# Kernel tuning notes

Measured on AMD Instinct MI355X. Metric: run time of the kernel, lower is better.

Reference implementation:

```python
import jax, jax.numpy as jnp
import numpy as np

MODEL_DIM = 1024
BATCH, SEQ = 4, 2048


def setup_inputs() -> dict:
    key = jax.random.key(0)
    kx, kq, kk, kv = jax.random.split(key, 4)
    s = 1.0 / np.sqrt(MODEL_DIM)
    return {
        "x": jax.random.normal(kx, (BATCH, SEQ, MODEL_DIM), dtype=jnp.float32),
        "Wq": jax.random.normal(kq, (MODEL_DIM, MODEL_DIM), dtype=jnp.float32) * s,
        "Wk": jax.random.normal(kk, (MODEL_DIM, MODEL_DIM), dtype=jnp.float32) * s,
        "Wv": jax.random.normal(kv, (MODEL_DIM, MODEL_DIM), dtype=jnp.float32) * s,
    }


def reference(x, Wq, Wk, Wv):
    # nn.Linear(d, d, bias=False): y = x @ W.T ; W stored [out, in]
    q = jnp.einsum("bsd,ed->bse", x, Wq)
    k = jnp.einsum("bsd,ed->bse", x, Wk)
    v = jnp.einsum("bsd,ed->bse", x, Wv)
    scores = jnp.einsum("bqd,bkd->bqk", q, k) / jnp.sqrt(jnp.float32(MODEL_DIM))
    attn = jax.nn.softmax(scores, axis=-1)
    return jnp.einsum("bqk,bkd->bqd", attn, v)
```

## Files before the change

kernel.cpp:

```cpp
#include <hip/hip_runtime.h>
#include <hip/hip_bf16.h>


typedef short bf16x8_t __attribute__((ext_vector_type(8)));
typedef float f32x4_t __attribute__((ext_vector_type(4)));
typedef unsigned short u16x8_t __attribute__((ext_vector_type(8)));

static __device__ __forceinline__ unsigned short f2bf(float f) {
  __hip_bfloat16 h = __float2bfloat16(f);
  return *reinterpret_cast<unsigned short*>(&h);
}
static __device__ __forceinline__ float bf2f(unsigned short u) {
  return __uint_as_float(((unsigned int)u) << 16);
}

#define GLOAD_LDS16(gp, lp)                                            \
  __builtin_amdgcn_global_load_lds(                                    \
      (const __attribute__((address_space(1))) void*)(gp),             \
      (__attribute__((address_space(3))) void*)(lp), 16, 0, 0)

__global__ __launch_bounds__(256) void cast_f32_bf16(
    const float* __restrict__ in, unsigned short* __restrict__ out, int n8) {
  int i = blockIdx.x * 256 + threadIdx.x;
  if (i >= n8) return;
  float4 a = ((const float4*)in)[i * 2];
  float4 b = ((const float4*)in)[i * 2 + 1];
  u16x8_t o;
  o[0] = f2bf(a.x);
  o[1] = f2bf(a.y);
  o[2] = f2bf(a.z);
  o[3] = f2bf(a.w);
  o[4] = f2bf(b.x);
  o[5] = f2bf(b.y);
  o[6] = f2bf(b.z);
  o[7] = f2bf(b.w);
  ((u16x8_t*)out)[i] = o;
}

template <bool OUT_BF16, int BN>
__global__ __launch_bounds__(256) void gemm_nt(
    const unsigned short* __restrict__ A, const unsigned short* __restrict__ B,
    void* __restrict__ Cv, int M, int N, int K, int lda, int ldb, int ldc,
    long long sA, long long sB, long long sC, float alpha) {
  constexpr int NB = BN / 32;
  __shared__ unsigned short As[128 * 64];
  __shared__ unsigned short Bs[BN * 64];

  const int gx = gridDim.x, gy = gridDim.y;
  const int nwg = gx * gy * gridDim.z;
  const int orig = (blockIdx.z * gy + blockIdx.y) * gx + blockIdx.x;
  const int swz = (orig & 7) * (nwg >> 3) + (orig >> 3);
  const int bx = swz % gx;
  const int tmp = swz / gx;
  const int by = tmp % gy;
  const int z = tmp / gy;

  const int tid = threadIdx.x;
  const int lane = tid & 63;
  const int w = tid >> 6;
  const int wm = w >> 1, wn = w & 1;
  const int m0 = by * 128;
  const int n0 = bx * BN;

  A += (long long)z * sA;
  B += (long long)z * sB;

  int sarow[4], sacol[4];
#pragma unroll
  for (int i = 0; i < 4; ++i) {
    int p = w * 256 + i * 64 + lane;
    int r = p >> 3;
    int c8 = (p & 7) ^ (r & 7);
    sarow[i] = r;
    sacol[i] = c8 * 8;
  }
  int sbrow[NB], sbcol[NB];
#pragma unroll
  for (int i = 0; i < NB; ++i) {
    int p = w * (BN * 2) + i * 64 + lane;
    int r = p >> 3;
    int c8 = (p & 7) ^ (r & 7);
    sbrow[i] = r;
    sbcol[i] = c8 * 8;
  }

  const int q = lane >> 4, rl = lane & 15;
  int aoff[4][2], boff[NB][2];
#pragma unroll
  for (int t = 0; t < 4; ++t) {
#pragma unroll
    for (int ks = 0; ks < 2; ++ks) {
      int ra = wm * 64 + t * 16 + rl;
      int ca = ks * 4 + q;
      aoff[t][ks] = ra * 64 + ((ca ^ (ra & 7)) * 8);
    }
  }
#pragma unroll
  for (int u = 0; u < NB; ++u) {
#pragma unroll
    for (int ks = 0; ks < 2; ++ks) {
      int rb = wn * (BN / 2) + u * 16 + rl;
      int ca = ks * 4 + q;
      boff[u][ks] = rb * 64 + ((ca ^ (rb & 7)) * 8);
    }
  }

  f32x4_t acc[4][NB];
#pragma unroll
  for (int i = 0; i < 4; ++i)
#pragma unroll
    for (int j = 0; j < NB; ++j) acc[i][j] = (f32x4_t){0.f, 0.f, 0.f, 0.f};

  for (int k0 = 0; k0 < K; k0 += 64) {
    __syncthreads();
#pragma unroll
    for (int i = 0; i < 4; ++i) {
      GLOAD_LDS16(&A[(long long)(m0 + sarow[i]) * lda + k0 + sacol[i]],
                  &As[(w * 4 + i) * 512]);
    }
#pragma unroll
    for (int i = 0; i < NB; ++i) {
      GLOAD_LDS16(&B[(long long)(n0 + sbrow[i]) * ldb + k0 + sbcol[i]],
                  &Bs[(w * NB + i) * 512]);
    }
    __syncthreads();

#pragma unroll
    for (int ks = 0; ks < 2; ++ks) {
      bf16x8_t af[4], bg[NB];
#pragma unroll
      for (int t = 0; t < 4; ++t) af[t] = *(const bf16x8_t*)&As[aoff[t][ks]];
#pragma unroll
      for (int u = 0; u < NB; ++u) bg[u] = *(const bf16x8_t*)&Bs[boff[u][ks]];
#pragma unroll
      for (int i = 0; i < 4; ++i)
#pragma unroll
        for (int j = 0; j < NB; ++j)
          acc[i][j] = __builtin_amdgcn_mfma_f32_16x16x32_bf16(af[i], bg[j],
                                                              acc[i][j], 0, 0, 0);
    }
  }

  if (OUT_BF16) {
    unsigned short* C = (unsigned short*)Cv + (long long)z * sC;
#pragma unroll
    for (int t = 0; t < 4; ++t)
#pragma unroll
      for (int u = 0; u < NB; ++u)
#pragma unroll
        for (int j = 0; j < 4; ++j) {
          int row = m0 + wm * 64 + t * 16 + q * 4 + j;
          int col = n0 + wn * (BN / 2) + u * 16 + rl;
          C[(long long)row * ldc + col] = f2bf(acc[t][u][j] * alpha);
        }
  } else {
    float* C = (float*)Cv + (long long)z * sC;
#pragma unroll
    for (int t = 0; t < 4; ++t)
#pragma unroll
      for (int u = 0; u < NB; ++u)
#pragma unroll
        for (int j = 0; j < 4; ++j) {
          int row = m0 + wm * 64 + t * 16 + q * 4 + j;
          int col = n0 + wn * (BN / 2) + u * 16 + rl;
          C[(long long)row * ldc + col] = acc[t][u][j] * alpha;
        }
  }
}

__global__ __launch_bounds__(256) void softmax_bf16(
    unsigned short* __restrict__ S) {
  unsigned short* p = S + (long long)blockIdx.x * 2048;
  const int tid = threadIdx.x;

  u16x8_t v = ((u16x8_t*)p)[tid];
  float f[8];
#pragma unroll
  for (int j = 0; j < 8; ++j) f[j] = bf2f(v[j]);

  float m = f[0];
#pragma unroll
  for (int j = 1; j < 8; ++j) m = fmaxf(m, f[j]);
#pragma unroll
  for (int off = 32; off > 0; off >>= 1) m = fmaxf(m, __shfl_xor(m, off));

  __shared__ float redm[4];
  __shared__ float reds[4];
  if ((tid & 63) == 0) redm[tid >> 6] = m;
  __syncthreads();
  m = fmaxf(fmaxf(redm[0], redm[1]), fmaxf(redm[2], redm[3]));

  float s = 0.f;
#pragma unroll
  for (int j = 0; j < 8; ++j) {
    f[j] = __expf(f[j] - m);
    s += f[j];
  }
#pragma unroll
  for (int off = 32; off > 0; off >>= 1) s += __shfl_xor(s, off);
  if ((tid & 63) == 0) reds[tid >> 6] = s;
  __syncthreads();
  s = (reds[0] + reds[1]) + (reds[2] + reds[3]);

  const float inv = 1.0f / s;
#pragma unroll
  for (int j = 0; j < 8; ++j) v[j] = f2bf(f[j] * inv);
  ((u16x8_t*)p)[tid] = v;
}

extern "C" void kernel_launch(void* const* d_in, const int* in_sizes, int n_in,
                              void* d_out, int out_size, void* d_ws,
                              size_t ws_size, hipStream_t stream) {
  const float* x = (const float*)d_in[0];
  const float* Wq = (const float*)d_in[1];
  const float* Wk = (const float*)d_in[2];
  const float* Wv = (const float*)d_in[3];
  float* out = (float*)d_out;

  unsigned short* xb = (unsigned short*)d_ws;
  unsigned short* Wqb = xb + 8388608;
  unsigned short* Wkb = Wqb + 1048576;
  unsigned short* Wvb = Wkb + 1048576;
  unsigned short* Qb = Wvb + 1048576;
  unsigned short* Kb = Qb + 8388608;
  unsigned short* VTb = Kb + 8388608;
  unsigned short* Scb = VTb + 8388608;

  const dim3 blk(256);

  cast_f32_bf16<<<4096, blk, 0, stream>>>(x, xb, 1048576);
  cast_f32_bf16<<<512, blk, 0, stream>>>(Wq, Wqb, 131072);
  cast_f32_bf16<<<512, blk, 0, stream>>>(Wk, Wkb, 131072);
  cast_f32_bf16<<<512, blk, 0, stream>>>(Wv, Wvb, 131072);

  gemm_nt<true, 128><<<dim3(8, 64, 2), blk, 0, stream>>>(
      xb, Wqb, Qb, 8192, 1024, 1024, 1024, 1024, 1024, 0, 1048576,
      8388608, 1.0f);
  gemm_nt<true, 128><<<dim3(64, 8, 1), blk, 0, stream>>>(
      Wvb, xb, VTb, 1024, 8192, 1024, 1024, 1024, 8192, 0, 0, 0, 1.0f);

  gemm_nt<true, 128><<<dim3(16, 16, 4), blk, 0, stream>>>(
      Qb, Kb, Scb, 2048, 2048, 1024, 1024, 1024, 2048, (long long)2048 * 1024,
      (long long)2048 * 1024, (long long)2048 * 2048, 0.03125f);

  softmax_bf16<<<8192, blk, 0, stream>>>(Scb);

  gemm_nt<false, 64><<<dim3(16, 16, 4), blk, 0, stream>>>(
      Scb, VTb, out, 2048, 1024, 2048, 2048, 8192, 1024,
      (long long)2048 * 2048, 2048, (long long)2048 * 1024, 1.0f);
}
```

Measured before the change: 194.6 us.

## Fuse softmax into QK^T epilogue, batch Q/K projection, add 256-tile double-buffered GEMM

Drops the separate softmax kernel. The QK^T GEMM epilogue now writes exp(scores) as bf16 and atomically adds row sums, and the PV GEMM divides by those sums. Q and K projections are merged into one 256x256-tile GEMM with a concatenated weight matrix, and the three weight casts are merged into one launch. The new GEMM uses 512 threads with a two-stage global-to-LDS pipeline and MFMA priority hints. The risk is that softmax no longer subtracts the row max, so exp can overflow for inputs with large scores. It also adds float atomics on the row sums.

```diff
diff --git a/kernel.cpp b/kernel.cpp
--- a/kernel.cpp
+++ b/kernel.cpp
@@ -9,9 +9,6 @@
 static __device__ __forceinline__ unsigned short f2bf(float f) {
   __hip_bfloat16 h = __float2bfloat16(f);
   return *reinterpret_cast<unsigned short*>(&h);
-}
-static __device__ __forceinline__ float bf2f(unsigned short u) {
-  return __uint_as_float(((unsigned int)u) << 16);
 }
 
 #define GLOAD_LDS16(gp, lp)                                            \
@@ -26,25 +23,41 @@
   float4 a = ((const float4*)in)[i * 2];
   float4 b = ((const float4*)in)[i * 2 + 1];
   u16x8_t o;
-  o[0] = f2bf(a.x);
-  o[1] = f2bf(a.y);
-  o[2] = f2bf(a.z);
-  o[3] = f2bf(a.w);
-  o[4] = f2bf(b.x);
-  o[5] = f2bf(b.y);
-  o[6] = f2bf(b.z);
-  o[7] = f2bf(b.w);
+  o[0] = f2bf(a.x); o[1] = f2bf(a.y); o[2] = f2bf(a.z); o[3] = f2bf(a.w);
+  o[4] = f2bf(b.x); o[5] = f2bf(b.y); o[6] = f2bf(b.z); o[7] = f2bf(b.w);
   ((u16x8_t*)out)[i] = o;
 }
 
-template <bool OUT_BF16, int BN>
-__global__ __launch_bounds__(256) void gemm_nt(
+__global__ __launch_bounds__(256) void cast_w3(
+    const float* __restrict__ Wq, const float* __restrict__ Wk,
+    const float* __restrict__ Wv, unsigned short* __restrict__ Wqk,
+    unsigned short* __restrict__ Wvb) {
+  int i = blockIdx.x * 256 + threadIdx.x;
+  int seg = i >> 17;
+  int local = i & 131071;
+  const float* src = (seg == 0) ? Wq : ((seg == 1) ? Wk : Wv);
+  unsigned short* dst =
+      (seg == 0) ? Wqk : ((seg == 1) ? (Wqk + 1048576) : Wvb);
+  float4 a = ((const float4*)src)[local * 2];
+  float4 b = ((const float4*)src)[local * 2 + 1];
+  u16x8_t o;
+  o[0] = f2bf(a.x); o[1] = f2bf(a.y); o[2] = f2bf(a.z); o[3] = f2bf(a.w);
+  o[4] = f2bf(b.x); o[5] = f2bf(b.y); o[6] = f2bf(b.z); o[7] = f2bf(b.w);
+  ((u16x8_t*)dst)[local] = o;
+}
+
+__global__ __launch_bounds__(256) void zero_f32(float* __restrict__ p, int n) {
+  int i = blockIdx.x * 256 + threadIdx.x;
+  if (i < n) p[i] = 0.0f;
+}
+
+template <int EPI>
+__global__ __launch_bounds__(512, 2) void gemm256_nt(
     const unsigned short* __restrict__ A, const unsigned short* __restrict__ B,
-    void* __restrict__ Cv, int M, int N, int K, int lda, int ldb, int ldc,
-    long long sA, long long sB, long long sC, float alpha) {
-  constexpr int NB = BN / 32;
-  __shared__ unsigned short As[128 * 64];
-  __shared__ unsigned short Bs[BN * 64];
+    unsigned short* __restrict__ C, float* __restrict__ rowsum, int K,
+    int lda, int ldb, int ldc, long long sA, long long sB, long long sC,
+    float alpha, int rsz) {
+  __shared__ unsigned short lds[2][2][256 * 64];
 
   const int gx = gridDim.x, gy = gridDim.y;
   const int nwg = gx * gy * gridDim.z;
@@ -58,6 +71,149 @@
   const int tid = threadIdx.x;
   const int lane = tid & 63;
   const int w = tid >> 6;
+  const int wm = w >> 2, wn = w & 3;
+  const int m0 = by * 256, n0 = bx * 256;
+
+  A += (long long)z * sA;
+  B += (long long)z * sB;
+
+  int sar[4], sac[4];
+#pragma unroll
+  for (int i = 0; i < 4; ++i) {
+    int p = i * 512 + w * 64 + lane;
+    int r = p >> 3;
+    sar[i] = r;
+    sac[i] = ((p & 7) ^ (r & 7)) * 8;
+  }
+
+  const int q = lane >> 4, rl = lane & 15;
+  int aoff[8][2], boff[4][2];
+#pragma unroll
+  for (int t = 0; t < 8; ++t)
+#pragma unroll
+    for (int ks = 0; ks < 2; ++ks) {
+      int ra = wm * 128 + t * 16 + rl;
+      int ca = ks * 4 + q;
+      aoff[t][ks] = ra * 64 + ((ca ^ (ra & 7)) * 8);
+    }
+#pragma unroll
+  for (int u = 0; u < 4; ++u)
+#pragma unroll
+    for (int ks = 0; ks < 2; ++ks) {
+      int rb = wn * 64 + u * 16 + rl;
+      int ca = ks * 4 + q;
+      boff[u][ks] = rb * 64 + ((ca ^ (rb & 7)) * 8);
+    }
+
+  f32x4_t acc[8][4];
+#pragma unroll
+  for (int i = 0; i < 8; ++i)
+#pragma unroll
+    for (int j = 0; j < 4; ++j) acc[i][j] = (f32x4_t){0.f, 0.f, 0.f, 0.f};
+
+#define STAGE256(bufi, k0)                                                   \
+  {                                                                          \
+    _Pragma("unroll") for (int i = 0; i < 4; ++i)                            \
+        GLOAD_LDS16(&A[(long long)(m0 + sar[i]) * lda + (k0) + sac[i]],      \
+                    &lds[bufi][0][(i * 512 + w * 64) * 8]);                  \
+    _Pragma("unroll") for (int i = 0; i < 4; ++i)                            \
+        GLOAD_LDS16(&B[(long long)(n0 + sar[i]) * ldb + (k0) + sac[i]],      \
+                    &lds[bufi][1][(i * 512 + w * 64) * 8]);                  \
+  }
+
+  const int NT = K >> 6;
+  STAGE256(0, 0);
+  STAGE256(1, 64);
+
+  for (int t = 0; t < NT; ++t) {
+    const int cur = t & 1;
+    if (t < NT - 1)
+      asm volatile("s_waitcnt vmcnt(8)" ::: "memory");
+    else
+      asm volatile("s_waitcnt vmcnt(0)" ::: "memory");
+    __builtin_amdgcn_s_barrier();
+    __builtin_amdgcn_sched_barrier(0);
+    const unsigned short* Al = &lds[cur][0][0];
+    const unsigned short* Bl = &lds[cur][1][0];
+#pragma unroll
+    for (int ks = 0; ks < 2; ++ks) {
+      bf16x8_t af[8], bg[4];
+#pragma unroll
+      for (int tt = 0; tt < 8; ++tt)
+        af[tt] = *(const bf16x8_t*)&Al[aoff[tt][ks]];
+#pragma unroll
+      for (int u = 0; u < 4; ++u) bg[u] = *(const bf16x8_t*)&Bl[boff[u][ks]];
+      __builtin_amdgcn_s_setprio(1);
+#pragma unroll
+      for (int i = 0; i < 8; ++i)
+#pragma unroll
+        for (int j = 0; j < 4; ++j)
+          acc[i][j] = __builtin_amdgcn_mfma_f32_16x16x32_bf16(af[i], bg[j],
+                                                              acc[i][j], 0, 0, 0);
+      __builtin_amdgcn_s_setprio(0);
+    }
+    __builtin_amdgcn_sched_barrier(0);
+    __builtin_amdgcn_s_barrier();
+    __builtin_amdgcn_sched_barrier(0);
+    if (t + 2 < NT) STAGE256(cur, (t + 2) * 64);
+  }
+
+  if (EPI == 0) {
+#pragma unroll
+    for (int tt = 0; tt < 8; ++tt)
+#pragma unroll
+      for (int u = 0; u < 4; ++u)
+#pragma unroll
+        for (int j = 0; j < 4; ++j) {
+          int row = m0 + wm * 128 + tt * 16 + q * 4 + j;
+          int col = n0 + wn * 64 + u * 16 + rl;
+          C[(long long)z * sC + (long long)row * ldc + col] =
+              f2bf(acc[tt][u][j] * alpha);
+        }
+  } else {
+#pragma unroll
+    for (int tt = 0; tt < 8; ++tt)
+#pragma unroll
+      for (int j = 0; j < 4; ++j) {
+        int row = m0 + wm * 128 + tt * 16 + q * 4 + j;
+        float sum = 0.f;
+#pragma unroll
+        for (int u = 0; u < 4; ++u) {
+          float e = __expf(acc[tt][u][j] * alpha);
+          int col = n0 + wn * 64 + u * 16 + rl;
+          C[(long long)z * sC + (long long)row * ldc + col] = f2bf(e);
+          sum += e;
+        }
+#pragma unroll
+        for (int mk = 1; mk <= 8; mk <<= 1) sum += __shfl_xor(sum, mk);
+        if (rl == 0) atomicAdd(&rowsum[z * rsz + row], sum);
+      }
+  }
+#undef STAGE256
+}
+
+template <int EPI, int BN>
+__global__ __launch_bounds__(256) void gemm_nt(
+    const unsigned short* __restrict__ A, const unsigned short* __restrict__ B,
+    void* __restrict__ Cv, const float* __restrict__ rowsum, int M, int N,
+    int K, int lda, int ldb, int ldc, long long sA, long long sB,
+    long long sC, float alpha, int rsz) {
+  constexpr int NB = BN / 32;
+  __shared__ unsigned short As[128 * 64];
+  __shared__ unsigned short Bs[BN * 64];
+
+  const int gx = gridDim.x, gy = gridDim.y;
+  const int nwg = gx * gy * gridDim.z;
+  const int orig = (blockIdx.z * gy + blockIdx.y) * gx + blockIdx.x;
+  const int swz = (orig & 7) * (nwg >> 3) + (orig >> 3);
+  const int bx = swz % gx;
+  const int tmp = swz / gx;
+  const int by = tmp % gy;
+  const int z = tmp / gy;
+
+  const int tid = threadIdx.x;
+  const int lane = tid & 63;
+  const int w = tid >> 6;
   const int wm = w >> 1, wn = w & 1;
   const int m0 = by * 128;
   const int n0 = bx * BN;
@@ -70,40 +226,36 @@
   for (int i = 0; i < 4; ++i) {
     int p = w * 256 + i * 64 + lane;
     int r = p >> 3;
-    int c8 = (p & 7) ^ (r & 7);
     sarow[i] = r;
-    sacol[i] = c8 * 8;
+    sacol[i] = ((p & 7) ^ (r & 7)) * 8;
   }
   int sbrow[NB], sbcol[NB];
 #pragma unroll
   for (int i = 0; i < NB; ++i) {
     int p = w * (BN * 2) + i * 64 + lane;
     int r = p >> 3;
-    int c8 = (p & 7) ^ (r & 7);
     sbrow[i] = r;
-    sbcol[i] = c8 * 8;
+    sbcol[i] = ((p & 7) ^ (r & 7)) * 8;
   }
 
   const int q = lane >> 4, rl = lane & 15;
   int aoff[4][2], boff[NB][2];
 #pragma unroll
-  for (int t = 0; t < 4; ++t) {
+  for (int t = 0; t < 4; ++t)
 #pragma unroll
     for (int ks = 0; ks < 2; ++ks) {
       int ra = wm * 64 + t * 16 + rl;
       int ca = ks * 4 + q;
       aoff[t][ks] = ra * 64 + ((ca ^ (ra & 7)) * 8);
     }
-  }
-#pragma unroll
-  for (int u = 0; u < NB; ++u) {
+#pragma unroll
+  for (int u = 0; u < NB; ++u)
 #pragma unroll
     for (int ks = 0; ks < 2; ++ks) {
       int rb = wn * (BN / 2) + u * 16 + rl;
       int ca = ks * 4 + q;
       boff[u][ks] = rb * 64 + ((ca ^ (rb & 7)) * 8);
     }
-  }
 
   f32x4_t acc[4][NB];
 #pragma unroll
@@ -141,71 +293,26 @@
     }
   }
 
-  if (OUT_BF16) {
-    unsigned short* C = (unsigned short*)Cv + (long long)z * sC;
-#pragma unroll
-    for (int t = 0; t < 4; ++t)
-#pragma unroll
-      for (int u = 0; u < NB; ++u)
-#pragma unroll
-        for (int j = 0; j < 4; ++j) {
-          int row = m0 + wm * 64 + t * 16 + q * 4 + j;
-          int col = n0 + wn * (BN / 2) + u * 16 + rl;
-          C[(long long)row * ldc + col] = f2bf(acc[t][u][j] * alpha);
+#pragma unroll
+  for (int t = 0; t < 4; ++t)
+#pragma unroll
+    for (int u = 0; u < NB; ++u)
+#pragma unroll
+      for (int j = 0; j < 4; ++j) {
+        int row = m0 + wm * 64 + t * 16 + q * 4 + j;
+        int col = n0 + wn * (BN / 2) + u * 16 + rl;
+        if (EPI == 0) {
+          ((unsigned short*)Cv)[(long long)z * sC + (long long)row * ldc +
+                                col] = f2bf(acc[t][u][j] * alpha);
+        } else if (EPI == 1) {
+          ((float*)Cv)[(long long)z * sC + (long long)row * ldc + col] =
+              acc[t][u][j] * alpha;
+        } else {
+          float inv = 1.0f / rowsum[z * rsz + row];
+          ((float*)Cv)[(long long)z * sC + (long long)row * ldc + col] =
+              acc[t][u][j] * inv;
         }
-  } else {
-    float* C = (float*)Cv + (long long)z * sC;
-#pragma unroll
-    for (int t = 0; t < 4; ++t)
-#pragma unroll
-      for (int u = 0; u < NB; ++u)
-#pragma unroll
-        for (int j = 0; j < 4; ++j) {
-          int row = m0 + wm * 64 + t * 16 + q * 4 + j;
-          int col = n0 + wn * (BN / 2) + u * 16 + rl;
-          C[(long long)row * ldc + col] = acc[t][u][j] * alpha;
-        }
-  }
-}
-
-__global__ __launch_bounds__(256) void softmax_bf16(
-    unsigned short* __restrict__ S) {
-  unsigned short* p = S + (long long)blockIdx.x * 2048;
-  const int tid = threadIdx.x;
-
-  u16x8_t v = ((u16x8_t*)p)[tid];
-  float f[8];
-#pragma unroll
-  for (int j = 0; j < 8; ++j) f[j] = bf2f(v[j]);
-
-  float m = f[0];
-#pragma unroll
-  for (int j = 1; j < 8; ++j) m = fmaxf(m, f[j]);
-#pragma unroll
-  for (int off = 32; off > 0; off >>= 1) m = fmaxf(m, __shfl_xor(m, off));
-
-  __shared__ float redm[4];
-  __shared__ float reds[4];
-  if ((tid & 63) == 0) redm[tid >> 6] = m;
-  __syncthreads();
-  m = fmaxf(fmaxf(redm[0], redm[1]), fmaxf(redm[2], redm[3]));
-
-  float s = 0.f;
-#pragma unroll
-  for (int j = 0; j < 8; ++j) {
-    f[j] = __expf(f[j] - m);
-    s += f[j];
-  }
-#pragma unroll
-  for (int off = 32; off > 0; off >>= 1) s += __shfl_xor(s, off);
-  if ((tid & 63) == 0) reds[tid >> 6] = s;
-  __syncthreads();
-  s = (reds[0] + reds[1]) + (reds[2] + reds[3]);
-
-  const float inv = 1.0f / s;
-#pragma unroll
-  for (int j = 0; j < 8; ++j) v[j] = f2bf(f[j] * inv);
-  ((u16x8_t*)p)[tid] = v;
+      }
 }
 
 extern "C" void kernel_launch(void* const* d_in, const int* in_sizes, int n_in,
@@ -218,34 +325,33 @@
   float* out = (float*)d_out;
 
   unsigned short* xb = (unsigned short*)d_ws;
-  unsigned short* Wqb = xb + 8388608;
-  unsigned short* Wkb = Wqb + 1048576;
-  unsigned short* Wvb = Wkb + 1048576;
-  unsigned short* Qb = Wvb + 1048576;
-  unsigned short* Kb = Qb + 8388608;
-  unsigned short* VTb = Kb + 8388608;
+  unsigned short* Wqk = xb + 8388608;
+  unsigned short* Wvb = Wqk + 2097152;
+  unsigned short* Cqk = Wvb + 1048576;
+  unsigned short* VTb = Cqk + 16777216;
   unsigned short* Scb = VTb + 8388608;
+  float* rowsumf = (float*)(Scb + 16777216);
 
   const dim3 blk(256);
+  const dim3 blk512(512);
 
   cast_f32_bf16<<<4096, blk, 0, stream>>>(x, xb, 1048576);
-  cast_f32_bf16<<<512, blk, 0, stream>>>(Wq, Wqb, 131072);
-  cast_f32_bf16<<<512, blk, 0, stream>>>(Wk, Wkb, 131072);
-  cast_f32_bf16<<<512, blk, 0, stream>>>(Wv, Wvb, 131072);
-
-  gemm_nt<true, 128><<<dim3(8, 64, 2), blk, 0, stream>>>(
-      xb, Wqb, Qb, 8192, 1024, 1024, 1024, 1024, 1024, 0, 1048576,
-      8388608, 1.0f);
-  gemm_nt<true, 128><<<dim3(64, 8, 1), blk, 0, stream>>>(
-      Wvb, xb, VTb, 1024, 8192, 1024, 1024, 1024, 8192, 0, 0, 0, 1.0f);
-
-  gemm_nt<true, 128><<<dim3(16, 16, 4), blk, 0, stream>>>(
-      Qb, Kb, Scb, 2048, 2048, 1024, 1024, 1024, 2048, (long long)2048 * 1024,
-      (long long)2048 * 1024, (long long)2048 * 2048, 0.03125f);
-
-  softmax_bf16<<<8192, blk, 0, stream>>>(Scb);
-
-  gemm_nt<false, 64><<<dim3(16, 16, 4), blk, 0, stream>>>(
-      Scb, VTb, out, 2048, 1024, 2048, 2048, 8192, 1024,
-      (long long)2048 * 2048, 2048, (long long)2048 * 1024, 1.0f);
-}
+  cast_w3<<<1536, blk, 0, stream>>>(Wq, Wk, Wv, Wqk, Wvb);
+  zero_f32<<<32, blk, 0, stream>>>(rowsumf, 8192);
+
+  gemm256_nt<0><<<dim3(8, 32, 1), blk512, 0, stream>>>(
+      xb, Wqk, Cqk, nullptr, 1024, 1024, 1024, 2048, 0, 0, 0, 1.0f, 0);
+
+  gemm_nt<0, 128><<<dim3(64, 8, 1), blk, 0, stream>>>(
+      Wvb, xb, VTb, nullptr, 1024, 8192, 1024, 1024, 1024, 8192, 0, 0, 0,
+      1.0f, 0);
+
+  gemm256_nt<1><<<dim3(8, 8, 4), blk512, 0, stream>>>(
+      Cqk, Cqk + 1024, Scb, rowsumf, 1024, 2048, 2048, 2048,
+      (long long)2048 * 2048, (long long)2048 * 2048, (long long)2048 * 2048,
+      0.03125f, 2048);
+
+  gemm_nt<2, 64><<<dim3(16, 16, 4), blk, 0, stream>>>(
+      Scb, VTb, out, rowsumf, 2048, 1024, 2048, 2048, 8192, 1024,
+      (long long)2048 * 2048, 2048, (long long)2048 * 1024, 1.0f, 2048);
+}
```

Result: faster. 169.7 us (-12.8%).
